# Performance work log

Measured on AMD Instinct MI355X. Metric: run time of the kernel, lower is better.

## Reference

```python
import jax, jax.numpy as jnp
import numpy as np

N_GRAPHS = 16
NPG = 420               # nodes per graph (fc1 expects 420*64 flatten)
N = N_GRAPHS * NPG      # 6720
DEG = 8
E = N * DEG             # 53760
HEADS = 4
IN_DIM = 2048
C1 = 1024               # per-head channels, layer 1
C2 = 64                 # layer 2 channels
OUT_DIM = 18
SLOPE = 0.2             # GATConv leaky_relu negative_slope


def _seg_softmax(scores, idx, n):
    # numerically-stable softmax over edges grouped by destination node
    m = jax.lax.stop_gradient(jax.ops.segment_max(scores, idx, num_segments=n))
    ex = jnp.exp(scores - m[idx])
    den = jax.ops.segment_sum(ex, idx, num_segments=n)
    return ex / (den[idx] + 1e-16)


def _transformer_conv(x, src, dst, wq, bq, wk, bk, wv, bv, ws, bs, heads, ch):
    # PyG TransformerConv defaults: concat=True, beta=False, root_weight=True, dropout=0
    n = x.shape[0]
    q = (x @ wq + bq).reshape(n, heads, ch)
    k = (x @ wk + bk).reshape(n, heads, ch)
    v = (x @ wv + bv).reshape(n, heads, ch)
    alpha = jnp.einsum('ehc,ehc->eh', q[dst], k[src]) / (ch ** 0.5)  # [E,H]
    alpha = _seg_softmax(alpha, dst, n)
    out = jax.ops.segment_sum(v[src] * alpha[..., None], dst, num_segments=n)  # [N,H,C]
    return out.reshape(n, heads * ch) + (x @ ws + bs)  # skip connection (lin_skip)


def _gat_conv(x, src, dst, w, a_src, a_dst, bias, heads, ch, concat):
    # PyG GATConv defaults: add_self_loops=True, negative_slope=0.2, lin has no bias
    n = x.shape[0]
    loop = jnp.arange(n, dtype=src.dtype)
    s = jnp.concatenate([src, loop])
    d = jnp.concatenate([dst, loop])
    h = (x @ w).reshape(n, heads, ch)
    es = jnp.einsum('nhc,hc->nh', h, a_src)
    ed = jnp.einsum('nhc,hc->nh', h, a_dst)
    e = jax.nn.leaky_relu(es[s] + ed[d], SLOPE)  # [E+N, H]
    alpha = _seg_softmax(e, d, n)
    out = jax.ops.segment_sum(h[s] * alpha[..., None], d, num_segments=n)  # [N,H,C]
    out = out.reshape(n, heads * ch) if concat else out.mean(axis=1)
    return out + bias


def setup_inputs() -> dict:
    key = jax.random.key(0)
    it = iter(jax.random.split(key, 64))
    def nrm(shape, scale):
        return jax.random.normal(next(it), shape, jnp.float32) * scale
    def lin(fi, fo):
        return nrm((fi, fo), float(1.0 / np.sqrt(fi)))
    p = {}
    p['x'] = nrm((N, IN_DIM), 1.0)
    p['edge_index'] = jax.random.randint(next(it), (2, E), 0, N, dtype=jnp.int32)
    for nm in ['t1_wq', 't1_wk', 't1_wv', 't1_ws']:
        p[nm] = lin(IN_DIM, HEADS * C1)
    for nm in ['t1_bq', 't1_bk', 't1_bv', 't1_bs']:
        p[nm] = jnp.zeros((HEADS * C1,), jnp.float32)
    # TransformerConv 2: 4096 -> 64, 1 head
    for nm in ['t2_wq', 't2_wk', 't2_wv', 't2_ws']:
        p[nm] = lin(HEADS * C1, C2)
    for nm in ['t2_bq', 't2_bk', 't2_bv', 't2_bs']:
        p[nm] = jnp.zeros((C2,), jnp.float32)
    p['g1_w'] = lin(IN_DIM, HEADS * C1)
    p['g1_as'] = nrm((HEADS, C1), 0.02)
    p['g1_ad'] = nrm((HEADS, C1), 0.02)
    p['g1_b'] = jnp.zeros((HEADS * C1,), jnp.float32)
    # GATConv 2: 4096 -> 64, 1 head, concat=False (mean)
    p['g2_w'] = lin(HEADS * C1, C2)
    p['g2_as'] = nrm((1, C2), 0.02)
    p['g2_ad'] = nrm((1, C2), 0.02)
    p['g2_b'] = jnp.zeros((C2,), jnp.float32)
    # MLP head
    p['fc1_w'] = lin(NPG * C2, 256); p['fc1_b'] = jnp.zeros((256,), jnp.float32)
    p['fc2_w'] = lin(256, 128);      p['fc2_b'] = jnp.zeros((128,), jnp.float32)
    p['fc3_w'] = lin(128, 64);       p['fc3_b'] = jnp.zeros((64,), jnp.float32)
    p['fc4_w'] = lin(64, OUT_DIM);   p['fc4_b'] = jnp.zeros((OUT_DIM,), jnp.float32)
    return p


def _forward(edge_index, x,
             t1_wq, t1_bq, t1_wk, t1_bk, t1_wv, t1_bv, t1_ws, t1_bs,
             t2_wq, t2_bq, t2_wk, t2_bk, t2_wv, t2_bv, t2_ws, t2_bs,
             g1_w, g1_as, g1_ad, g1_b, g2_w, g2_as, g2_ad, g2_b,
             fc1_w, fc1_b, fc2_w, fc2_b, fc3_w, fc3_b, fc4_w, fc4_b):
    src, dst = edge_index[0], edge_index[1]
    h = jax.nn.relu(_transformer_conv(x, src, dst, t1_wq, t1_bq, t1_wk, t1_bk,
                                      t1_wv, t1_bv, t1_ws, t1_bs, HEADS, C1))
    h = jax.nn.relu(_transformer_conv(h, src, dst, t2_wq, t2_bq, t2_wk, t2_bk,
                                      t2_wv, t2_bv, t2_ws, t2_bs, 1, C2))
    z = jax.nn.relu(_gat_conv(x, src, dst, g1_w, g1_as, g1_ad, g1_b, HEADS, C1, True))
    z = jax.nn.relu(_gat_conv(z, src, dst, g2_w, g2_as, g2_ad, g2_b, 1, C2, False))
    s = (h + z).reshape(-1, NPG * C2)          # [n_graphs, 26880]
    s = jax.nn.relu(s @ fc1_w + fc1_b)          # dropout = identity at eval
    s = jax.nn.relu(s @ fc2_w + fc2_b)
    s = jax.nn.relu(s @ fc3_w + fc3_b)
    return s @ fc4_w + fc4_b                    # [n_graphs, OUT_DIM]


def reference(x, edge_index,
              t1_wq, t1_bq, t1_wk, t1_bk, t1_wv, t1_bv, t1_ws, t1_bs,
              t2_wq, t2_bq, t2_wk, t2_bk, t2_wv, t2_bv, t2_ws, t2_bs,
              g1_w, g1_as, g1_ad, g1_b, g2_w, g2_as, g2_ad, g2_b,
              fc1_w, fc1_b, fc2_w, fc2_b, fc3_w, fc3_b, fc4_w, fc4_b):
    return _forward(edge_index, x,
                    t1_wq, t1_bq, t1_wk, t1_bk, t1_wv, t1_bv, t1_ws, t1_bs,
                    t2_wq, t2_bq, t2_wk, t2_bk, t2_wv, t2_bv, t2_ws, t2_bs,
                    g1_w, g1_as, g1_ad, g1_b, g2_w, g2_as, g2_ad, g2_b,
                    fc1_w, fc1_b, fc2_w, fc2_b, fc3_w, fc3_b, fc4_w, fc4_b)
```

## Files before the change

### kernel.cpp

```cpp
#include <hip/hip_runtime.h>
#include <stdint.h>
#include <stdio.h>

#define NNODES 6720
#define NEDGES 53760
#define NGRAPH 16
#define INDIM  2048
#define HEADS1 4
#define C1DIM  1024
#define D1     4096
#define C2DIM  64
#define N2     320
#define OUTDIM 18

typedef unsigned short u16;
typedef unsigned int   u32;

__device__ __forceinline__ float b2f(u16 u) {
  union { float f; u32 u; } v; v.u = ((u32)u) << 16; return v.f;
}
__device__ __forceinline__ u16 f2b(float f) {
  union { float f; u32 u; } v; v.f = f;
  u32 r = v.u + 0x7FFFu + ((v.u >> 16) & 1u);
  return (u16)(r >> 16);
}
__device__ __forceinline__ float ldf(const void* p, long i, int isf) {
  return isf ? ((const float*)p)[i] : b2f(((const u16*)p)[i]);
}

typedef __attribute__((ext_vector_type(8))) short bf16x8;
typedef __attribute__((ext_vector_type(4))) float f32x4;

__device__ __forceinline__ void gld_lds16(const u16* g, u16* l) {
  __builtin_amdgcn_global_load_lds((const __attribute__((address_space(1))) void*)g,
                                   (__attribute__((address_space(3))) void*)l, 16, 0, 0);
}

__global__ void detect_dtype(const u16* __restrict__ x, int* flag) {
  __shared__ int cnt;
  if (threadIdx.x == 0) cnt = 0;
  __syncthreads();
  int c = 0;
  for (int i = threadIdx.x; i < 4096; i += 256) {
    u16 u = x[2 * i];
    int e = (u >> 7) & 0xFF;
    if (e >= 118 && e <= 135) c++;
  }
  atomicAdd(&cnt, c);
  __syncthreads();
  if (threadIdx.x == 0) *flag = (cnt > 2048) ? 0 : 1;
}

__global__ void conv_any(const void* __restrict__ src, u16* __restrict__ dst,
                         long n, const int* __restrict__ flag) {
  long i = (long)blockIdx.x * 256 + threadIdx.x;
  long stride = (long)gridDim.x * 256;
  int isf = *flag;
  if (isf) {
    const float* s = (const float*)src;
    for (long j = i; j < n; j += stride) dst[j] = f2b(s[j]);
  } else {
    const u16* s = (const u16*)src;
    for (long j = i; j < n; j += stride) dst[j] = s[j];
  }
}

#define NSMALL 13
struct SmallConv {
  const void* src[NSMALL];
  u16*        dst[NSMALL];
  int         n[NSMALL];
};
__global__ void conv_small(SmallConv sc, const int* __restrict__ flag) {
  int b = blockIdx.x;
  int isf = *flag;
  const void* s = sc.src[b];
  u16* d = sc.dst[b];
  int n = sc.n[b];
  if (isf) {
    const float* sf = (const float*)s;
    for (int i = threadIdx.x; i < n; i += 256) d[i] = f2b(sf[i]);
  } else {
    const u16* sb = (const u16*)s;
    for (int i = threadIdx.x; i < n; i += 256) d[i] = sb[i];
  }
}

__global__ __launch_bounds__(256) void transpose_any(const void* __restrict__ src,
                                                     u16* __restrict__ dst,
                                                     int K, int Ncols,
                                                     const int* __restrict__ flag) {
  __shared__ u16 tile[32][33];
  int isf = *flag;
  int tx = threadIdx.x & 31, ty = threadIdx.x >> 5;
  int c0 = blockIdx.x * 32, r0 = blockIdx.y * 32;
  if (isf) {
    const float* s = (const float*)src;
    #pragma unroll
    for (int i = 0; i < 32; i += 8)
      tile[ty + i][tx] = f2b(s[(long)(r0 + ty + i) * Ncols + c0 + tx]);
  } else {
    const u16* s = (const u16*)src;
    #pragma unroll
    for (int i = 0; i < 32; i += 8)
      tile[ty + i][tx] = s[(long)(r0 + ty + i) * Ncols + c0 + tx];
  }
  __syncthreads();
  #pragma unroll
  for (int i = 0; i < 32; i += 8)
    dst[(long)(c0 + ty + i) * K + r0 + tx] = tile[tx][ty + i];
}

__global__ void pack_bias(const void* bq1, const void* bk1, const void* bv1, const void* bs1,
                          const void* bq2, const void* bk2, const void* bv2, const void* bs2,
                          float* bias1, float* bias2, const int* flag) {
  int isf = *flag;
  int i = blockIdx.x * 256 + threadIdx.x;
  if (i < 20480) {
    float v = 0.f;
    if (i < 4096) v = ldf(bq1, i, isf);
    else if (i < 8192)  v = ldf(bk1, i - 4096, isf);
    else if (i < 12288) v = ldf(bv1, i - 8192, isf);
    else if (i < 16384) v = ldf(bs1, i - 12288, isf);
    bias1[i] = v;
  } else if (i < 20480 + N2) {
    int j = i - 20480; float v = 0.f;
    if (j < 64) v = ldf(bq2, j, isf);
    else if (j < 128) v = ldf(bk2, j - 64, isf);
    else if (j < 192) v = ldf(bv2, j - 128, isf);
    else if (j < 256) v = ldf(bs2, j - 192, isf);
    bias2[j] = v;
  }
}

__global__ __launch_bounds__(256) void gemm_bt_128(const u16* __restrict__ A,
                                                   const u16* __restrict__ BT,
                                                   const float* __restrict__ bias,
                                                   u16* __restrict__ C,
                                                   int M, int N, int K) {
  __shared__ u16 As[128 * 32];
  __shared__ u16 Bs[128 * 32];
  const int tid = threadIdx.x, lane = tid & 63, wave = tid >> 6;
  const int m0 = blockIdx.y * 128, n0 = blockIdx.x * 128;
  const int wm = (wave >> 1) * 64, wn = (wave & 1) * 64;

  const int srow = tid >> 2, scp = tid & 3;
  const int scl8 = (scp ^ ((srow >> 1) & 3)) * 8;
  int ar0 = m0 + srow;      if (ar0 >= M) ar0 = M - 1;
  int ar1 = m0 + srow + 64; if (ar1 >= M) ar1 = M - 1;
  const u16* ag0 = A + (long)ar0 * K + scl8;
  const u16* ag1 = A + (long)ar1 * K + scl8;
  const u16* bg0 = BT + (long)(n0 + srow) * K + scl8;
  const u16* bg1 = BT + (long)(n0 + srow + 64) * K + scl8;
  u16* al0 = As + tid * 8;
  u16* al1 = As + 2048 + tid * 8;
  u16* bl0 = Bs + tid * 8;
  u16* bl1 = Bs + 2048 + tid * 8;

  f32x4 acc[4][4];
  #pragma unroll
  for (int i = 0; i < 4; i++)
    #pragma unroll
    for (int j = 0; j < 4; j++) { f32x4 z = {0.f, 0.f, 0.f, 0.f}; acc[i][j] = z; }

  const int fr = lane & 15, q = lane >> 4;
  const int fq = (q ^ ((fr >> 1) & 3)) * 8;
  const u16* apA = As + (wm + fr) * 32 + fq;
  const u16* apB = Bs + (wn + fr) * 32 + fq;

  for (int k0 = 0; k0 < K; k0 += 32) {
    __syncthreads();
    gld_lds16(ag0 + k0, al0);
    gld_lds16(ag1 + k0, al1);
    gld_lds16(bg0 + k0, bl0);
    gld_lds16(bg1 + k0, bl1);
    __syncthreads();
    bf16x8 af[4], bfv[4];
    #pragma unroll
    for (int i = 0; i < 4; i++) af[i] = *(const bf16x8*)(apA + i * 16 * 32);
    #pragma unroll
    for (int j = 0; j < 4; j++) bfv[j] = *(const bf16x8*)(apB + j * 16 * 32);
    #pragma unroll
    for (int i = 0; i < 4; i++)
      #pragma unroll
      for (int j = 0; j < 4; j++)
        acc[i][j] = __builtin_amdgcn_mfma_f32_16x16x32_bf16(af[i], bfv[j], acc[i][j], 0, 0, 0);
  }

  const int q4 = (lane >> 4) * 4, cl = lane & 15;
  #pragma unroll
  for (int i = 0; i < 4; i++)
    #pragma unroll
    for (int r = 0; r < 4; r++) {
      int row = m0 + wm + i * 16 + q4 + r;
      if (row < M) {
        #pragma unroll
        for (int j = 0; j < 4; j++) {
          int col = n0 + wn + j * 16 + cl;
          C[(long)row * N + col] = f2b(acc[i][j][r] + bias[col]);
        }
      }
    }
}

__global__ __launch_bounds__(256) void gemm2_64(const u16* __restrict__ h1,
                                                const u16* __restrict__ z1,
                                                const u16* __restrict__ wt2,
                                                const float* __restrict__ bias2,
                                                u16* __restrict__ y2) {
  __shared__ u16 As[64 * 64];
  __shared__ u16 Bs[64 * 64];
  const int nt = blockIdx.x;
  const u16* A = (nt < 4) ? h1 : z1;
  const u16* BT = wt2 + (size_t)nt * 64 * D1;
  const int m0 = blockIdx.y * 64, n0 = nt * 64;
  const int tid = threadIdx.x, lane = tid & 63, wave = tid >> 6;

  const int sr = tid >> 3, cp = tid & 7;
  const int cgl8 = (cp ^ (sr & 7)) * 8;
  const u16* ag0 = A + (long)(m0 + sr) * D1 + cgl8;
  const u16* ag1 = ag0 + (long)32 * D1;
  const u16* bg0 = BT + (long)sr * D1 + cgl8;
  const u16* bg1 = bg0 + (long)32 * D1;
  u16* al0 = As + tid * 8;  u16* al1 = As + 2048 + tid * 8;
  u16* bl0 = Bs + tid * 8;  u16* bl1 = Bs + 2048 + tid * 8;

  f32x4 acc[4];
  #pragma unroll
  for (int j = 0; j < 4; j++) { f32x4 z = {0.f, 0.f, 0.f, 0.f}; acc[j] = z; }

  const int fr = lane & 15, q = lane >> 4;
  const int x0 = ((q)     ^ (fr & 7)) * 8;
  const int x1 = ((4 + q) ^ (fr & 7)) * 8;
  const u16* apA = As + (wave * 16 + fr) * 64;

  for (int k0 = 0; k0 < D1; k0 += 64) {
    __syncthreads();
    gld_lds16(ag0 + k0, al0);
    gld_lds16(ag1 + k0, al1);
    gld_lds16(bg0 + k0, bl0);
    gld_lds16(bg1 + k0, bl1);
    __syncthreads();
    bf16x8 a0 = *(const bf16x8*)(apA + x0);
    bf16x8 a1 = *(const bf16x8*)(apA + x1);
    #pragma unroll
    for (int j = 0; j < 4; j++) {
      bf16x8 b0 = *(const bf16x8*)(Bs + (j * 16 + fr) * 64 + x0);
      acc[j] = __builtin_amdgcn_mfma_f32_16x16x32_bf16(a0, b0, acc[j], 0, 0, 0);
    }
    #pragma unroll
    for (int j = 0; j < 4; j++) {
      bf16x8 b1 = *(const bf16x8*)(Bs + (j * 16 + fr) * 64 + x1);
      acc[j] = __builtin_amdgcn_mfma_f32_16x16x32_bf16(a1, b1, acc[j], 0, 0, 0);
    }
  }
  const int q4 = (lane >> 4) * 4, cl = lane & 15;
  #pragma unroll
  for (int j = 0; j < 4; j++)
    #pragma unroll
    for (int r = 0; r < 4; r++) {
      int row = m0 + wave * 16 + q4 + r;
      int col = n0 + j * 16 + cl;
      y2[(long)row * N2 + col] = f2b(acc[j][r] + bias2[col]);
    }
}

__global__ void zero_kernel(int* deg, float* f1sum) {
  int i = blockIdx.x * 256 + threadIdx.x;
  if (i < NNODES) deg[i] = 0;
  if (i < NGRAPH * 256) f1sum[i] = 0.f;
}

__global__ void count_deg(const int* __restrict__ ei, int* deg) {
  int e = blockIdx.x * 256 + threadIdx.x;
  if (e < NEDGES) atomicAdd(&deg[ei[NEDGES + e]], 1);
}

__global__ __launch_bounds__(1024) void scan_deg(const int* __restrict__ deg, int* off, int* cur) {
  __shared__ int sh[1024];
  const int t = threadIdx.x;
  const int PER = 7;
  int base = t * PER;
  int loc[PER];
  int sum = 0;
  #pragma unroll
  for (int i = 0; i < PER; i++) {
    int v = (base + i < NNODES) ? deg[base + i] : 0;
    loc[i] = sum; sum += v;
  }
  sh[t] = sum;
  __syncthreads();
  for (int d = 1; d < 1024; d <<= 1) {
    int v = (t >= d) ? sh[t - d] : 0;
    __syncthreads();
    sh[t] += v;
    __syncthreads();
  }
  int prev = (t > 0) ? sh[t - 1] : 0;
  #pragma unroll
  for (int i = 0; i < PER; i++) {
    int idx = base + i;
    if (idx <= NNODES) {
      int v = prev + loc[i];
      off[idx] = v;
      if (idx < NNODES) cur[idx] = v;
    }
  }
}

__global__ void scatter_edges(const int* __restrict__ ei, int* cur,
                              int* esrc, int* edst) {
  int e = blockIdx.x * 256 + threadIdx.x;
  if (e < NEDGES) {
    int s = ei[e], d = ei[NEDGES + e];
    int p = atomicAdd(&cur[d], 1);
    esrc[p] = s; edst[p] = d;
  }
}

__global__ __launch_bounds__(256) void t1_score_csr(const u16* __restrict__ yqk,
                                                    const int* __restrict__ off,
                                                    const int* __restrict__ esrc,
                                                    float* __restrict__ sc) {
  __shared__ float qsh[4096];
  int n = blockIdx.x, tid = threadIdx.x, lane = tid & 63, wave = tid >> 6;
  const u16* qr = yqk + (long)n * 8192;
  for (int i = tid * 8; i < 4096; i += 2048) {
    uint4 qa = *(const uint4*)(qr + i);
    const u16* qs = (const u16*)&qa;
    #pragma unroll
    for (int j = 0; j < 8; j++) qsh[i + j] = b2f(qs[j]);
  }
  __syncthreads();
  int p0 = off[n], p1 = off[n + 1];
  for (int p = p0 + wave; p < p1; p += 4) {
    const u16* k = yqk + (long)esrc[p] * 8192 + 4096;
    float dot[HEADS1];
    #pragma unroll
    for (int h = 0; h < HEADS1; h++) dot[h] = 0.f;
    #pragma unroll
    for (int h = 0; h < HEADS1; h++) {
      #pragma unroll
      for (int c = 0; c < 2; c++) {
        int idx = h * C1DIM + c * 512 + lane * 8;
        uint4 ka = *(const uint4*)(k + idx);
        const u16* ks = (const u16*)&ka;
        #pragma unroll
        for (int i = 0; i < 8; i++) dot[h] += qsh[idx + i] * b2f(ks[i]);
      }
    }
    #pragma unroll
    for (int h = 0; h < HEADS1; h++) {
      float v = dot[h];
      #pragma unroll
      for (int o = 32; o > 0; o >>= 1) v += __shfl_xor(v, o, 64);
      if (lane == 0) sc[(long)p * HEADS1 + h] = v * (1.0f / 32.0f);
    }
  }
}

__global__ void seg_softmax(const int* __restrict__ off, float* __restrict__ sc,
                            float* __restrict__ selfsc, int heads, int useSelf) {
  int i = blockIdx.x * 256 + threadIdx.x;
  if (i >= NNODES * heads) return;
  int n = i / heads, h = i - n * heads;
  int p0 = off[n], p1 = off[n + 1];
  float m = -3.4e38f;
  for (int p = p0; p < p1; p++) m = fmaxf(m, sc[p * heads + h]);
  if (useSelf) m = fmaxf(m, selfsc[i]);
  float den = 0.f;
  for (int p = p0; p < p1; p++) {
    float e = __expf(sc[p * heads + h] - m);
    sc[p * heads + h] = e; den += e;
  }
  float selfe = 0.f;
  if (useSelf) { selfe = __expf(selfsc[i] - m); den += selfe; }
  float inv = 1.0f / (den + 1e-16f);
  for (int p = p0; p < p1; p++) sc[p * heads + h] *= inv;
  if (useSelf) selfsc[i] = selfe * inv;
}

__global__ __launch_bounds__(256) void t1_agg(const u16* __restrict__ yvs,
                                              const int* __restrict__ off,
                                              const int* __restrict__ esrc,
                                              const float* __restrict__ alpha,
                                              u16* __restrict__ h1) {
  int n = blockIdx.x, t = threadIdx.x, h = t >> 6;
  int p0 = off[n], p1 = off[n + 1];
  float acc[16];
  #pragma unroll
  for (int i = 0; i < 16; i++) acc[i] = 0.f;
  for (int p = p0; p < p1; p++) {
    float a = alpha[p * 4 + h];
    const u16* v = yvs + (long)esrc[p] * 8192 + t * 16;
    uint4 v0 = *(const uint4*)(v);
    uint4 v1 = *(const uint4*)(v + 8);
    const u16* s0 = (const u16*)&v0; const u16* s1 = (const u16*)&v1;
    #pragma unroll
    for (int i = 0; i < 8; i++) acc[i] += a * b2f(s0[i]);
    #pragma unroll
    for (int i = 0; i < 8; i++) acc[8 + i] += a * b2f(s1[i]);
  }
  const u16* sk = yvs + (long)n * 8192 + 4096 + t * 16;
  uint4 k0 = *(const uint4*)(sk); uint4 k1 = *(const uint4*)(sk + 8);
  const u16* ks0 = (const u16*)&k0; const u16* ks1 = (const u16*)&k1;
  u16 outv[16];
  #pragma unroll
  for (int i = 0; i < 8; i++) outv[i] = f2b(fmaxf(acc[i] + b2f(ks0[i]), 0.f));
  #pragma unroll
  for (int i = 0; i < 8; i++) outv[8 + i] = f2b(fmaxf(acc[8 + i] + b2f(ks1[i]), 0.f));
  *(uint4*)(h1 + (long)n * D1 + t * 16) = *(uint4*)outv;
  *(uint4*)(h1 + (long)n * D1 + t * 16 + 8) = *(uint4*)(outv + 8);
}

__global__ __launch_bounds__(256) void g1_dots(const u16* __restrict__ gat,
                                               const u16* __restrict__ a_src,
                                               const u16* __restrict__ a_dst,
                                               float* __restrict__ es, float* __restrict__ ed) {
  int n = blockIdx.x;
  int h = threadIdx.x >> 6, lane = threadIdx.x & 63;
  const u16* hr = gat + (long)n * D1 + h * C1DIM;
  const u16* as = a_src + h * C1DIM;
  const u16* ad = a_dst + h * C1DIM;
  float s1 = 0.f, s2 = 0.f;
  #pragma unroll
  for (int c = 0; c < 2; c++) {
    int idx = c * 512 + lane * 8;
    uint4 hv = *(const uint4*)(hr + idx);
    uint4 av = *(const uint4*)(as + idx);
    uint4 dv = *(const uint4*)(ad + idx);
    const u16* hs = (const u16*)&hv; const u16* a1 = (const u16*)&av; const u16* d1 = (const u16*)&dv;
    #pragma unroll
    for (int i = 0; i < 8; i++) {
      float x = b2f(hs[i]);
      s1 += x * b2f(a1[i]); s2 += x * b2f(d1[i]);
    }
  }
  #pragma unroll
  for (int o = 32; o > 0; o >>= 1) { s1 += __shfl_xor(s1, o, 64); s2 += __shfl_xor(s2, o, 64); }
  if (lane == 0) { es[n * 4 + h] = s1; ed[n * 4 + h] = s2; }
}

__global__ void gat_score(const int* __restrict__ esrc, const int* __restrict__ edst,
                          const float* __restrict__ es, const float* __restrict__ ed,
                          float* __restrict__ sc, float* __restrict__ selfsc, int heads) {
  int i = blockIdx.x * 256 + threadIdx.x;
  int ne = NEDGES * heads;
  if (i < ne) {
    int p = i / heads, h = i - p * heads;
    float v = es[esrc[p] * heads + h] + ed[edst[p] * heads + h];
    sc[i] = (v > 0.f) ? v : 0.2f * v;
  } else {
    int j = i - ne;
    if (j < NNODES * heads) {
      float v = es[j] + ed[j];
      selfsc[j] = (v > 0.f) ? v : 0.2f * v;
    }
  }
}

__global__ __launch_bounds__(256) void g1_agg(const u16* __restrict__ gat,
                                              const int* __restrict__ off,
                                              const int* __restrict__ esrc,
                                              const float* __restrict__ alpha,
                                              const float* __restrict__ selfa,
                                              const u16* __restrict__ bias,
                                              u16* __restrict__ z1) {
  int n = blockIdx.x, t = threadIdx.x, h = t >> 6;
  int p0 = off[n], p1 = off[n + 1];
  float acc[16];
  #pragma unroll
  for (int i = 0; i < 16; i++) acc[i] = 0.f;
  for (int p = p0; p < p1; p++) {
    float a = alpha[p * 4 + h];
    const u16* v = gat + (long)esrc[p] * D1 + t * 16;
    uint4 v0 = *(const uint4*)(v);
    uint4 v1 = *(const uint4*)(v + 8);
    const u16* s0 = (const u16*)&v0; const u16* s1 = (const u16*)&v1;
    #pragma unroll
    for (int i = 0; i < 8; i++) acc[i] += a * b2f(s0[i]);
    #pragma unroll
    for (int i = 0; i < 8; i++) acc[8 + i] += a * b2f(s1[i]);
  }
  {
    float a = selfa[n * 4 + h];
    const u16* v = gat + (long)n * D1 + t * 16;
    uint4 v0 = *(const uint4*)(v);
    uint4 v1 = *(const uint4*)(v + 8);
    const u16* s0 = (const u16*)&v0; const u16* s1 = (const u16*)&v1;
    #pragma unroll
    for (int i = 0; i < 8; i++) acc[i] += a * b2f(s0[i]);
    #pragma unroll
    for (int i = 0; i < 8; i++) acc[8 + i] += a * b2f(s1[i]);
  }
  u16 outv[16];
  #pragma unroll
  for (int i = 0; i < 16; i++) outv[i] = f2b(fmaxf(acc[i] + b2f(bias[t * 16 + i]), 0.f));
  *(uint4*)(z1 + (long)n * D1 + t * 16) = *(uint4*)outv;
  *(uint4*)(z1 + (long)n * D1 + t * 16 + 8) = *(uint4*)(outv + 8);
}

__global__ __launch_bounds__(256) void t2_score(const u16* __restrict__ y2,
                                                const int* __restrict__ esrc,
                                                const int* __restrict__ edst,
                                                float* __restrict__ sc) {
  int w = (blockIdx.x * 256 + threadIdx.x) >> 6, lane = threadIdx.x & 63;
  if (w >= NEDGES) return;
  float q = b2f(y2[(long)edst[w] * N2 + lane]);
  float k = b2f(y2[(long)esrc[w] * N2 + C2DIM + lane]);
  float v = q * k;
  #pragma unroll
  for (int o = 32; o > 0; o >>= 1) v += __shfl_xor(v, o, 64);
  if (lane == 0) sc[w] = v * 0.125f;
}

__global__ __launch_bounds__(256) void t2_agg(const u16* __restrict__ y2,
                                              const int* __restrict__ off,
                                              const int* __restrict__ esrc,
                                              const float* __restrict__ alpha,
                                              float* __restrict__ sn) {
  int n = (blockIdx.x * 256 + threadIdx.x) >> 6, lane = threadIdx.x & 63;
  if (n >= NNODES) return;
  int p0 = off[n], p1 = off[n + 1];
  float acc = 0.f;
  for (int p = p0; p < p1; p++)
    acc += alpha[p] * b2f(y2[(long)esrc[p] * N2 + 2 * C2DIM + lane]);
  acc += b2f(y2[(long)n * N2 + 3 * C2DIM + lane]);
  sn[(long)n * C2DIM + lane] = fmaxf(acc, 0.f);
}

__global__ __launch_bounds__(256) void g2_dots(const u16* __restrict__ y2,
                                               const u16* __restrict__ as,
                                               const u16* __restrict__ ad,
                                               float* __restrict__ es, float* __restrict__ ed) {
  int n = (blockIdx.x * 256 + threadIdx.x) >> 6, lane = threadIdx.x & 63;
  if (n >= NNODES) return;
  float x = b2f(y2[(long)n * N2 + 4 * C2DIM + lane]);
  float s1 = x * b2f(as[lane]), s2 = x * b2f(ad[lane]);
  #pragma unroll
  for (int o = 32; o > 0; o >>= 1) { s1 += __shfl_xor(s1, o, 64); s2 += __shfl_xor(s2, o, 64); }
  if (lane == 0) { es[n] = s1; ed[n] = s2; }
}

__global__ __launch_bounds__(256) void g2_agg(const u16* __restrict__ y2,
                                              const int* __restrict__ off,
                                              const int* __restrict__ esrc,
                                              const float* __restrict__ alpha,
                                              const float* __restrict__ selfa,
                                              const u16* __restrict__ bias,
                                              float* __restrict__ sn) {
  int n = (blockIdx.x * 256 + threadIdx.x) >> 6, lane = threadIdx.x & 63;
  if (n >= NNODES) return;
  int p0 = off[n], p1 = off[n + 1];
  float acc = 0.f;
  for (int p = p0; p < p1; p++)
    acc += alpha[p] * b2f(y2[(long)esrc[p] * N2 + 4 * C2DIM + lane]);
  acc += selfa[n] * b2f(y2[(long)n * N2 + 4 * C2DIM + lane]);
  float v = fmaxf(acc + b2f(bias[lane]), 0.f);
  sn[(long)n * C2DIM + lane] += v;
}

#define FCHUNK 210
__global__ __launch_bounds__(256) void fc1_partial(const float* __restrict__ sn,
                                                   const void* __restrict__ w,
                                                   const int* __restrict__ flag,
                                                   float* __restrict__ f1sum) {
  __shared__ float sl[16 * FCHUNK];
  int k0 = blockIdx.x * FCHUNK;
  int t = threadIdx.x;
  int isf = *flag;
  for (int idx = t; idx < 16 * FCHUNK; idx += 256) {
    int g = idx / FCHUNK, kk = idx - g * FCHUNK;
    sl[idx] = sn[(long)g * 26880 + k0 + kk];
  }
  __syncthreads();
  float acc[16];
  #pragma unroll
  for (int g = 0; g < 16; g++) acc[g] = 0.f;
  if (isf) {
    const float* wf = (const float*)w;
    for (int kk = 0; kk < FCHUNK; kk++) {
      float wv = wf[(long)(k0 + kk) * 256 + t];
      #pragma unroll
      for (int g = 0; g < 16; g++) acc[g] += sl[g * FCHUNK + kk] * wv;
    }
  } else {
    const u16* wb = (const u16*)w;
    for (int kk = 0; kk < FCHUNK; kk++) {
      float wv = b2f(wb[(long)(k0 + kk) * 256 + t]);
      #pragma unroll
      for (int g = 0; g < 16; g++) acc[g] += sl[g * FCHUNK + kk] * wv;
    }
  }
  #pragma unroll
  for (int g = 0; g < 16; g++) atomicAdd(&f1sum[g * 256 + t], acc[g]);
}

__global__ __launch_bounds__(256) void fc_tail(const float* __restrict__ f1sum,
                                               const u16* b1, const u16* w2, const u16* b2,
                                               const u16* w3, const u16* b3,
                                               const u16* w4, const u16* b4,
                                               void* __restrict__ out,
                                               const int* __restrict__ flag) {
  __shared__ float A1[16 * 256];
  __shared__ float A2[16 * 128];
  __shared__ float A3[16 * 64];
  int isf = *flag;
  int t = threadIdx.x;
  for (int i = t; i < 4096; i += 256) A1[i] = fmaxf(f1sum[i] + b2f(b1[i & 255]), 0.f);
  __syncthreads();
  for (int i = t; i < 2048; i += 256) {
    int g = i >> 7, j = i & 127;
    float acc = b2f(b2[j]);
    for (int k = 0; k < 256; k++) acc += A1[g * 256 + k] * b2f(w2[k * 128 + j]);
    A2[i] = fmaxf(acc, 0.f);
  }
  __syncthreads();
  for (int i = t; i < 1024; i += 256) {
    int g = i >> 6, j = i & 63;
    float acc = b2f(b3[j]);
    for (int k = 0; k < 128; k++) acc += A2[g * 128 + k] * b2f(w3[k * 64 + j]);
    A3[i] = fmaxf(acc, 0.f);
  }
  __syncthreads();
  for (int i = t; i < NGRAPH * OUTDIM; i += 256) {
    int g = i / OUTDIM, j = i - g * OUTDIM;
    float acc = b2f(b4[j]);
    for (int k = 0; k < 64; k++) acc += A3[g * 64 + k] * b2f(w4[k * OUTDIM + j]);
    if (isf) ((float*)out)[i] = acc;
    else     ((u16*)out)[i] = f2b(acc);
  }
}

extern "C" void kernel_launch(void* const* d_in, const int* in_sizes, int n_in,
                              void* d_out, int out_size, void* d_ws, size_t ws_size,
                              hipStream_t stream) {
  const void* x     = d_in[0];
  const int*  ei    = (const int*)d_in[1];
  const void* t1_wq = d_in[2];
  const void* t1_wk = d_in[3];
  const void* t1_wv = d_in[4];
  const void* t1_ws = d_in[5];
  const void* t1_bq = d_in[6];
  const void* t1_bk = d_in[7];
  const void* t1_bv = d_in[8];
  const void* t1_bs = d_in[9];
  const void* t2_wq = d_in[10];
  const void* t2_wk = d_in[11];
  const void* t2_wv = d_in[12];
  const void* t2_ws = d_in[13];
  const void* t2_bq = d_in[14];
  const void* t2_bk = d_in[15];
  const void* t2_bv = d_in[16];
  const void* t2_bs = d_in[17];
  const void* g1_w  = d_in[18];
  const void* g1_as = d_in[19];
  const void* g1_ad = d_in[20];
  const void* g1_b  = d_in[21];
  const void* g2_w  = d_in[22];
  const void* g2_as = d_in[23];
  const void* g2_ad = d_in[24];
  const void* g2_b  = d_in[25];
  const void* fc1_w = d_in[26];
  const void* fc1_b = d_in[27];
  const void* fc2_w = d_in[28];
  const void* fc2_b = d_in[29];
  const void* fc3_w = d_in[30];
  const void* fc3_b = d_in[31];
  const void* fc4_w = d_in[32];
  const void* fc4_b = d_in[33];

  char* wp = (char*)d_ws;
  auto alloc = [&](size_t bytes) {
    char* p = wp; wp += (bytes + 255) & ~(size_t)255; return p;
  };
  u16*   wtSlab = (u16*)  alloc((size_t)8192 * INDIM * 2);
  u16*   wt2    = (u16*)  alloc((size_t)N2 * D1 * 2);
  u16*   yqk    = (u16*)  alloc((size_t)NNODES * 8192 * 2);
  u16*   h1     = (u16*)  alloc((size_t)NNODES * D1 * 2);
  u16*   y2     = (u16*)  alloc((size_t)NNODES * N2 * 2);
  u16*   xb     = (u16*)  alloc((size_t)NNODES * INDIM * 2);
  u16*   fc2wb  = (u16*)  alloc((size_t)256 * 128 * 2);
  u16*   fc3wb  = (u16*)  alloc((size_t)128 * 64 * 2);
  u16*   fc4wb  = (u16*)  alloc((size_t)64 * OUTDIM * 2);
  u16*   fb1    = (u16*)  alloc(256 * 2);
  u16*   fb2    = (u16*)  alloc(128 * 2);
  u16*   fb3    = (u16*)  alloc(64 * 2);
  u16*   fb4    = (u16*)  alloc(OUTDIM * 2);
  u16*   g1asb  = (u16*)  alloc(4096 * 2);
  u16*   g1adb  = (u16*)  alloc(4096 * 2);
  u16*   g1bb   = (u16*)  alloc(4096 * 2);
  u16*   g2asb  = (u16*)  alloc(64 * 2);
  u16*   g2adb  = (u16*)  alloc(64 * 2);
  u16*   g2bb   = (u16*)  alloc(64 * 2);
  float* bias1  = (float*)alloc((size_t)20480 * 4);
  float* bias2  = (float*)alloc((size_t)N2 * 4);
  int*   flag   = (int*)  alloc(256);
  int*   deg    = (int*)  alloc((size_t)NNODES * 4);
  int*   off    = (int*)  alloc((size_t)(NNODES + 1) * 4);
  int*   cur    = (int*)  alloc((size_t)NNODES * 4);
  int*   esrc   = (int*)  alloc((size_t)NEDGES * 4);
  int*   edst   = (int*)  alloc((size_t)NEDGES * 4);
  float* scT1   = (float*)alloc((size_t)NEDGES * 4 * 4);
  float* esG1   = (float*)alloc((size_t)NNODES * 4 * 4);
  float* edG1   = (float*)alloc((size_t)NNODES * 4 * 4);
  float* scG1   = (float*)alloc((size_t)NEDGES * 4 * 4);
  float* sfG1   = (float*)alloc((size_t)NNODES * 4 * 4);
  float* scT2   = (float*)alloc((size_t)NEDGES * 4);
  float* scG2   = (float*)alloc((size_t)NEDGES * 4);
  float* sfG2   = (float*)alloc((size_t)NNODES * 4);
  float* es2    = (float*)alloc((size_t)NNODES * 4);
  float* ed2    = (float*)alloc((size_t)NNODES * 4);
  float* sn     = (float*)alloc((size_t)NNODES * C2DIM * 4);
  float* f1sum  = (float*)alloc((size_t)NGRAPH * 256 * 4);

  u16* gat = yqk;
  u16* z1  = yqk + (size_t)NNODES * D1;

  size_t need = (size_t)(wp - (char*)d_ws);
  if (ws_size < need) {
    fprintf(stderr, "[GATGT kernel] WORKSPACE TOO SMALL ws=%zu need=%zu\n", ws_size, need);
    return;
  }

  detect_dtype<<<1, 256, 0, stream>>>((const u16*)x, flag);

  zero_kernel<<<27, 256, 0, stream>>>(deg, f1sum);
  count_deg<<<NEDGES / 256, 256, 0, stream>>>(ei, deg);
  scan_deg<<<1, 1024, 0, stream>>>(deg, off, cur);
  scatter_edges<<<NEDGES / 256, 256, 0, stream>>>(ei, cur, esrc, edst);
  pack_bias<<<82, 256, 0, stream>>>(t1_bq, t1_bk, t1_bv, t1_bs,
                                    t2_bq, t2_bk, t2_bv, t2_bs, bias1, bias2, flag);

  conv_any<<<4096, 256, 0, stream>>>(x, xb, (long)NNODES * INDIM, flag);
  {
    SmallConv sc;
    const void* srcs[NSMALL] = { fc2_w, fc3_w, fc4_w, fc1_b, fc2_b, fc3_b, fc4_b,
                                 g1_as, g1_ad, g1_b, g2_as, g2_ad, g2_b };
    u16* dsts[NSMALL] = { fc2wb, fc3wb, fc4wb, fb1, fb2, fb3, fb4,
                          g1asb, g1adb, g1bb, g2asb, g2adb, g2bb };
    int  ns[NSMALL]   = { 256 * 128, 128 * 64, 64 * OUTDIM, 256, 128, 64, OUTDIM,
                          4096, 4096, 4096, 64, 64, 64 };
    for (int i = 0; i < NSMALL; i++) { sc.src[i] = srcs[i]; sc.dst[i] = dsts[i]; sc.n[i] = ns[i]; }
    conv_small<<<NSMALL, 256, 0, stream>>>(sc, flag);
  }

  transpose_any<<<dim3(128, 64), 256, 0, stream>>>(t1_wq, wtSlab, INDIM, 4096, flag);
  transpose_any<<<dim3(128, 64), 256, 0, stream>>>(t1_wk, wtSlab + (size_t)4096 * INDIM, INDIM, 4096, flag);
  gemm_bt_128<<<dim3(64, 53), 256, 0, stream>>>(xb, wtSlab, bias1, yqk, NNODES, 8192, INDIM);
  t1_score_csr<<<NNODES, 256, 0, stream>>>(yqk, off, esrc, scT1);
  seg_softmax<<<105, 256, 0, stream>>>(off, scT1, nullptr, 4, 0);

  transpose_any<<<dim3(128, 64), 256, 0, stream>>>(t1_wv, wtSlab, INDIM, 4096, flag);
  transpose_any<<<dim3(128, 64), 256, 0, stream>>>(t1_ws, wtSlab + (size_t)4096 * INDIM, INDIM, 4096, flag);
  gemm_bt_128<<<dim3(64, 53), 256, 0, stream>>>(xb, wtSlab, bias1 + 8192, yqk, NNODES, 8192, INDIM);
  t1_agg<<<NNODES, 256, 0, stream>>>(yqk, off, esrc, scT1, h1);

  transpose_any<<<dim3(128, 64), 256, 0, stream>>>(g1_w, wtSlab, INDIM, 4096, flag);
  gemm_bt_128<<<dim3(32, 53), 256, 0, stream>>>(xb, wtSlab, bias1 + 16384, gat, NNODES, 4096, INDIM);
  g1_dots<<<NNODES, 256, 0, stream>>>(gat, g1asb, g1adb, esG1, edG1);
  gat_score<<<(NEDGES * 4 + NNODES * 4 + 255) / 256, 256, 0, stream>>>(
      esrc, edst, esG1, edG1, scG1, sfG1, 4);
  seg_softmax<<<105, 256, 0, stream>>>(off, scG1, sfG1, 4, 1);
  g1_agg<<<NNODES, 256, 0, stream>>>(gat, off, esrc, scG1, sfG1, g1bb, z1);

  {
    const void* srcs2[5] = { t2_wq, t2_wk, t2_wv, t2_ws, g2_w };
    for (int s = 0; s < 5; s++)
      transpose_any<<<dim3(2, 128), 256, 0, stream>>>(
          srcs2[s], wt2 + (size_t)s * 64 * D1, D1, 64, flag);
  }
  gemm2_64<<<dim3(5, NNODES / 64), 256, 0, stream>>>(h1, z1, wt2, bias2, y2);

  t2_score<<<NEDGES / 4, 256, 0, stream>>>(y2, esrc, edst, scT2);
  seg_softmax<<<(NNODES + 255) / 256, 256, 0, stream>>>(off, scT2, nullptr, 1, 0);
  t2_agg<<<NNODES / 4, 256, 0, stream>>>(y2, off, esrc, scT2, sn);

  g2_dots<<<NNODES / 4, 256, 0, stream>>>(y2, g2asb, g2adb, es2, ed2);
  gat_score<<<(NEDGES + NNODES + 255) / 256, 256, 0, stream>>>(
      esrc, edst, es2, ed2, scG2, sfG2, 1);
  seg_softmax<<<(NNODES + 255) / 256, 256, 0, stream>>>(off, scG2, sfG2, 1, 1);
  g2_agg<<<NNODES / 4, 256, 0, stream>>>(y2, off, esrc, scG2, sfG2, g2bb, sn);

  fc1_partial<<<128, 256, 0, stream>>>(sn, fc1_w, flag, f1sum);
  fc_tail<<<1, 256, 0, stream>>>(f1sum, fb1, fc2wb, fb2, fc3wb, fb3,
                                 fc4wb, fb4, d_out, flag);
}
```

Measured before the change: 1.590 ms.

## Pipeline big GEMM with 4-stage LDS ring buffer and XCD-aware block remap

```diff
diff --git a/kernel.cpp b/kernel.cpp
--- a/kernel.cpp
+++ b/kernel.cpp
@@ -133,15 +133,25 @@
   }
 }
 
-__global__ __launch_bounds__(256) void gemm_bt_128(const u16* __restrict__ A,
-                                                   const u16* __restrict__ BT,
-                                                   const float* __restrict__ bias,
-                                                   u16* __restrict__ C,
-                                                   int M, int N, int K) {
-  __shared__ u16 As[128 * 32];
-  __shared__ u16 Bs[128 * 32];
+__global__ __launch_bounds__(256) void gemm_bt_r4(const u16* __restrict__ A,
+                                                  const u16* __restrict__ BT,
+                                                  const float* __restrict__ bias,
+                                                  u16* __restrict__ C,
+                                                  int M, int N, int K) {
+  __shared__ u16 As[4][128 * 32];
+  __shared__ u16 Bs[4][128 * 32];
+
+  const int nbx = gridDim.x;
+  const int nwg = nbx * gridDim.y;
+  const int orig = blockIdx.y * nbx + blockIdx.x;
+  const int xcd = orig & 7, rest = orig >> 3;
+  const int q8 = nwg >> 3, r8 = nwg & 7;
+  const int wg = (xcd < r8) ? (xcd * (q8 + 1) + rest)
+                            : (r8 * (q8 + 1) + (xcd - r8) * q8 + rest);
+  const int by = wg / nbx, bx = wg - by * nbx;
+
   const int tid = threadIdx.x, lane = tid & 63, wave = tid >> 6;
-  const int m0 = blockIdx.y * 128, n0 = blockIdx.x * 128;
+  const int m0 = by * 128, n0 = bx * 128;
   const int wm = (wave >> 1) * 64, wn = (wave & 1) * 64;
 
   const int srow = tid >> 2, scp = tid & 3;
@@ -152,10 +162,6 @@
   const u16* ag1 = A + (long)ar1 * K + scl8;
   const u16* bg0 = BT + (long)(n0 + srow) * K + scl8;
   const u16* bg1 = BT + (long)(n0 + srow + 64) * K + scl8;
-  u16* al0 = As + tid * 8;
-  u16* al1 = As + 2048 + tid * 8;
-  u16* bl0 = Bs + tid * 8;
-  u16* bl1 = Bs + 2048 + tid * 8;
 
   f32x4 acc[4][4];
   #pragma unroll
@@ -165,26 +171,47 @@
 
   const int fr = lane & 15, q = lane >> 4;
   const int fq = (q ^ ((fr >> 1) & 3)) * 8;
-  const u16* apA = As + (wm + fr) * 32 + fq;
-  const u16* apB = Bs + (wn + fr) * 32 + fq;
-
-  for (int k0 = 0; k0 < K; k0 += 32) {
-    __syncthreads();
-    gld_lds16(ag0 + k0, al0);
-    gld_lds16(ag1 + k0, al1);
-    gld_lds16(bg0 + k0, bl0);
-    gld_lds16(bg1 + k0, bl1);
-    __syncthreads();
+  const int aoff = (wm + fr) * 32 + fq;
+  const int boff = (wn + fr) * 32 + fq;
+
+  const int NT = K >> 5;
+
+  auto STAGE = [&](int t) {
+    const int b = t & 3;
+    const long k0 = (long)t * 32;
+    gld_lds16(ag0 + k0, &As[b][(size_t)tid * 8]);
+    gld_lds16(ag1 + k0, &As[b][2048 + (size_t)tid * 8]);
+    gld_lds16(bg0 + k0, &Bs[b][(size_t)tid * 8]);
+    gld_lds16(bg1 + k0, &Bs[b][2048 + (size_t)tid * 8]);
+  };
+
+  STAGE(0); STAGE(1); STAGE(2);
+
+  for (int t = 0; t < NT; ++t) {
+    if (t < NT - 2) {
+      asm volatile("s_waitcnt vmcnt(8)\n\ts_barrier" ::: "memory");
+    } else if (t == NT - 2) {
+      asm volatile("s_waitcnt vmcnt(4)\n\ts_barrier" ::: "memory");
+    } else {
+      asm volatile("s_waitcnt vmcnt(0)\n\ts_barrier" ::: "memory");
+    }
+    if (t + 3 < NT) STAGE(t + 3);
+
+    const u16* ab = &As[t & 3][0];
+    const u16* bb = &Bs[t & 3][0];
     bf16x8 af[4], bfv[4];
     #pragma unroll
-    for (int i = 0; i < 4; i++) af[i] = *(const bf16x8*)(apA + i * 16 * 32);
-    #pragma unroll
-    for (int j = 0; j < 4; j++) bfv[j] = *(const bf16x8*)(apB + j * 16 * 32);
+    for (int i = 0; i < 4; i++) af[i]  = *(const bf16x8*)(ab + aoff + i * 512);
+    #pragma unroll
+    for (int j = 0; j < 4; j++) bfv[j] = *(const bf16x8*)(bb + boff + j * 512);
+
+    __builtin_amdgcn_s_setprio(1);
     #pragma unroll
     for (int i = 0; i < 4; i++)
       #pragma unroll
       for (int j = 0; j < 4; j++)
         acc[i][j] = __builtin_amdgcn_mfma_f32_16x16x32_bf16(af[i], bfv[j], acc[i][j], 0, 0, 0);
+    __builtin_amdgcn_s_setprio(0);
   }
 
   const int q4 = (lane >> 4) * 4, cl = lane & 15;
@@ -747,17 +774,17 @@
 
   transpose_any<<<dim3(128, 64), 256, 0, stream>>>(t1_wq, wtSlab, INDIM, 4096, flag);
   transpose_any<<<dim3(128, 64), 256, 0, stream>>>(t1_wk, wtSlab + (size_t)4096 * INDIM, INDIM, 4096, flag);
-  gemm_bt_128<<<dim3(64, 53), 256, 0, stream>>>(xb, wtSlab, bias1, yqk, NNODES, 8192, INDIM);
+  gemm_bt_r4<<<dim3(64, 53), 256, 0, stream>>>(xb, wtSlab, bias1, yqk, NNODES, 8192, INDIM);
   t1_score_csr<<<NNODES, 256, 0, stream>>>(yqk, off, esrc, scT1);
   seg_softmax<<<105, 256, 0, stream>>>(off, scT1, nullptr, 4, 0);
 
   transpose_any<<<dim3(128, 64), 256, 0, stream>>>(t1_wv, wtSlab, INDIM, 4096, flag);
   transpose_any<<<dim3(128, 64), 256, 0, stream>>>(t1_ws, wtSlab + (size_t)4096 * INDIM, INDIM, 4096, flag);
-  gemm_bt_128<<<dim3(64, 53), 256, 0, stream>>>(xb, wtSlab, bias1 + 8192, yqk, NNODES, 8192, INDIM);
+  gemm_bt_r4<<<dim3(64, 53), 256, 0, stream>>>(xb, wtSlab, bias1 + 8192, yqk, NNODES, 8192, INDIM);
   t1_agg<<<NNODES, 256, 0, stream>>>(yqk, off, esrc, scT1, h1);
 
   transpose_any<<<dim3(128, 64), 256, 0, stream>>>(g1_w, wtSlab, INDIM, 4096, flag);
-  gemm_bt_128<<<dim3(32, 53), 256, 0, stream>>>(xb, wtSlab, bias1 + 16384, gat, NNODES, 4096, INDIM);
+  gemm_bt_r4<<<dim3(32, 53), 256, 0, stream>>>(xb, wtSlab, bias1 + 16384, gat, NNODES, 4096, INDIM);
   g1_dots<<<NNODES, 256, 0, stream>>>(gat, g1asb, g1adb, esG1, edG1);
   gat_score<<<(NEDGES * 4 + NNODES * 4 + 255) / 256, 256, 0, stream>>>(
       esrc, edst, esG1, edG1, scG1, sfG1, 4);
```

Result: slower. 1.718 ms (+8.0%).
